# Kernel tuning notes

Hardware: AMD Instinct MI355X
Metric: run time of the kernel (lower is better)

The kernel has to match this reference:

```python
import jax, jax.numpy as jnp
import numpy as np

ALPHA = 0.5
NUM_NB = 8


def setup_inputs() -> dict:
    key = jax.random.key(0)
    k1, k2 = jax.random.split(key)
    pc1 = jax.random.normal(k1, (4, 3, 8192), dtype=jnp.float32)
    pred_flow = jax.random.normal(k2, (4, 3, 8192), dtype=jnp.float32)
    return {"pc1": pc1, "pred_flow": pred_flow}


def reference(pc1, pred_flow):
    # pc1, pred_flow: [B, 3, N] -> [B, N, 3]
    B, _, N = pc1.shape
    k = NUM_NB
    p = jnp.transpose(pc1, (0, 2, 1))         # [B, N, 3]
    f = jnp.transpose(pred_flow, (0, 2, 1))   # [B, N, 3]

    sq = jnp.sum(p * p, axis=-1)
    sqrdist = sq[:, :, None] + sq[:, None, :] - 2.0 * jnp.einsum('bnd,bmd->bnm', p, p)

    # k+1 smallest (sorted ascending), drop self (first column)
    neg_d, kidx = jax.lax.top_k(-sqrdist, k + 1)  # descending in -d == ascending in d
    dists = -neg_d[:, :, 1:]                      # [B, N, k]
    kidx = kidx[:, :, 1:]                         # [B, N, k]
    dists = jnp.maximum(dists, 0.0)

    # softmax over all N*k weights per batch
    w = jax.nn.softmax(jnp.exp(-dists / ALPHA).reshape(B, N * k), axis=1)
    w = w.reshape(B, N, k)

    # gather neighbor flows: [B, N, k, 3]
    grouped = jnp.take_along_axis(f[:, None, :, :],
                                  kidx[:, :, :, None],
                                  axis=2)
    diff = jnp.linalg.norm(grouped - f[:, :, None, :], axis=3)  # [B, N, k]
    diff_flow = (N * w * diff).sum(axis=2)                      # [B, N]
    return jnp.mean(diff_flow)
```

## Files before the change

kernel.cpp:

```cpp
#include <hip/hip_runtime.h>
#include <hip/hip_bf16.h>
#include <math.h>

#define BATCH 4
#define NQ 8192
#define KNB 8
#define K1 9
#define CAP 34
#define THSAMP 256
#define SPART 2
#define IDXMASK 8191u
#define KEYMASK 0xFFFFE000u
#define EPS_S 1e-3f

#define CHAIN9(KEY) { unsigned kk = (KEY); \
  _Pragma("unroll") \
  for (int j = 0; j < K1; ++j) { \
    unsigned lo = min(kk, nk[j]); unsigned hi = max(kk, nk[j]); \
    nk[j] = lo; kk = hi; } }

#define CHAIN8(KEY) { unsigned kk = (KEY); \
  _Pragma("unroll") \
  for (int j = 0; j < KNB; ++j) { \
    unsigned lo = min(kk, nk[j]); unsigned hi = max(kk, nk[j]); \
    nk[j] = lo; kk = hi; } }

#define DRAIN() { \
  for (int i = 0; i < cnt; ++i) { \
    int j = sbuf[base + i]; \
    float dx = qx - px[j], dy = qy - py[j], dz = qz - pz[j]; \
    float d = dx*dx + dy*dy + dz*dz; \
    unsigned key = (__float_as_uint(d) & KEYMASK) | (unsigned)j; \
    if (key < nk[K1-1]) CHAIN9(key); \
  } \
  cnt = 0; \
  if (nk[K1-1] != 0xFFFFFFFFu) { \
    float td = __uint_as_float(nk[K1-1] | 0x1FFFu); \
    thetaS = fminf(thetaS, 0.5f*(td - qq) + EPS_S); \
  } }

#define GPROC(SS, GIDX) { \
  if ((SS) <= thetaS) { sbuf[base + cnt] = (unsigned short)(GIDX); cnt++; } }

#define SCORE4(S0,S1,S2,S3, X,Y,Z,H) \
  float S0 = fmaf(nqx, X.x, fmaf(nqy, Y.x, fmaf(nqz, Z.x, H.x))); \
  float S1 = fmaf(nqx, X.y, fmaf(nqy, Y.y, fmaf(nqz, Z.y, H.y))); \
  float S2 = fmaf(nqx, X.z, fmaf(nqy, Y.z, fmaf(nqz, Z.z, H.z))); \
  float S3 = fmaf(nqx, X.w, fmaf(nqy, Y.w, fmaf(nqz, Z.w, H.w)));

__global__ __launch_bounds__(256) void theta_kernel(
    const float* __restrict__ pc, unsigned* __restrict__ thetaOut,
    float* __restrict__ hOut)
{
  __shared__ float swx[THSAMP], swy[THSAMP], swz[THSAMP];
  const int b = blockIdx.y, p = blockIdx.z;
  const int q = blockIdx.x * 256 + threadIdx.x;
  const float* __restrict__ px = pc + (size_t)b * 3 * NQ;
  const float* __restrict__ py = px + NQ;
  const float* __restrict__ pz = px + 2 * NQ;
  const int tid = threadIdx.x;
  const int si = tid * (NQ / THSAMP) + p * (NQ / THSAMP / SPART);
  swx[tid] = px[si]; swy[tid] = py[si]; swz[tid] = pz[si];
  __syncthreads();
  const float qx = px[q], qy = py[q], qz = pz[q];
  if (p == 0) hOut[b * NQ + q] = 0.5f * (qx*qx + qy*qy + qz*qz);
  unsigned nk[K1];
#pragma unroll
  for (int j = 0; j < K1; ++j) nk[j] = 0xFFFFFFFFu;
  for (int i = 0; i < THSAMP; ++i) {
    float dx = qx - swx[i], dy = qy - swy[i], dz = qz - swz[i];
    float d = dx * dx + dy * dy + dz * dz;
    CHAIN9(__float_as_uint(d));
  }
  thetaOut[(size_t)(b * NQ + q) * SPART + p] = nk[K1 - 1] | 0x1FFFu;
}

__global__ __launch_bounds__(256) void knn_kernel(
    const float* __restrict__ pc, const float* __restrict__ hB,
    const unsigned* __restrict__ thetaIn, unsigned* __restrict__ wsK,
    int P, int cpp)
{
  __shared__ unsigned short sbuf[256 * CAP];
  const int b = blockIdx.y;
  const int p = blockIdx.z;
  const int q = blockIdx.x * 256 + threadIdx.x;
  const float* __restrict__ px = pc + (size_t)b * 3 * NQ;
  const float* __restrict__ py = px + NQ;
  const float* __restrict__ pz = px + 2 * NQ;
  const float* __restrict__ ph = hB + (size_t)b * NQ;
  const float4* __restrict__ px4 = (const float4*)px;
  const float4* __restrict__ py4 = (const float4*)py;
  const float4* __restrict__ pz4 = (const float4*)pz;
  const float4* __restrict__ ph4 = (const float4*)ph;
  const float qx = px[q], qy = py[q], qz = pz[q];
  const float nqx = -qx, nqy = -qy, nqz = -qz;
  const float qq = qx*qx + qy*qy + qz*qz;

  uint2 th = ((const uint2*)thetaIn)[b * NQ + q];
  float thetaS = 0.5f * (__uint_as_float(min(th.x, th.y)) - qq) + EPS_S;

  unsigned nk[K1];
#pragma unroll
  for (int j = 0; j < K1; ++j) nk[j] = 0xFFFFFFFFu;

  const unsigned base = (unsigned)threadIdx.x * CAP;
  int cnt = 0;
  const int c0 = p * cpp;

  for (int t = 0; t < cpp; t += 16) {
    if (__any(cnt >= CAP - 16)) { DRAIN(); }
    const int ti = (c0 + t) >> 2;
    const float4 X0 = px4[ti],     X1 = px4[ti + 1], X2 = px4[ti + 2], X3 = px4[ti + 3];
    const float4 Y0 = py4[ti],     Y1 = py4[ti + 1], Y2 = py4[ti + 2], Y3 = py4[ti + 3];
    const float4 Z0 = pz4[ti],     Z1 = pz4[ti + 1], Z2 = pz4[ti + 2], Z3 = pz4[ti + 3];
    const float4 H0 = ph4[ti],     H1 = ph4[ti + 1], H2 = ph4[ti + 2], H3 = ph4[ti + 3];
    SCORE4(s0, s1, s2, s3, X0, Y0, Z0, H0);
    SCORE4(s4, s5, s6, s7, X1, Y1, Z1, H1);
    SCORE4(s8, s9, sa, sb, X2, Y2, Z2, H2);
    SCORE4(sc, sd, se, sf, X3, Y3, Z3, H3);
    const int g = c0 + t;
    GPROC(s0, g + 0);  GPROC(s1, g + 1);  GPROC(s2, g + 2);  GPROC(s3, g + 3);
    GPROC(s4, g + 4);  GPROC(s5, g + 5);  GPROC(s6, g + 6);  GPROC(s7, g + 7);
    GPROC(s8, g + 8);  GPROC(s9, g + 9);  GPROC(sa, g + 10); GPROC(sb, g + 11);
    GPROC(sc, g + 12); GPROC(sd, g + 13); GPROC(se, g + 14); GPROC(sf, g + 15);
  }
  DRAIN();

#pragma unroll
  for (int j = 0; j < K1; ++j)
    wsK[((size_t)(b * P + p) * K1 + j) * NQ + q] = nk[j];
}

__global__ __launch_bounds__(64) void loss_kernel(
    const float* __restrict__ pc, const float* __restrict__ pf,
    const unsigned* __restrict__ wsK, float* __restrict__ acc,
    unsigned* __restrict__ doneCtr, float* __restrict__ out,
    int P, int nBlocks)
{
  const int b = blockIdx.y;
  const int q = blockIdx.x * 64 + threadIdx.x;
  const float* __restrict__ px = pc + (size_t)b * 3 * NQ;
  const float* __restrict__ py = px + NQ;
  const float* __restrict__ pz = px + 2 * NQ;
  const float* __restrict__ fx = pf + (size_t)b * 3 * NQ;
  const float* __restrict__ fy = fx + NQ;
  const float* __restrict__ fz = fx + 2 * NQ;

  unsigned nk[KNB];
#pragma unroll
  for (int j = 0; j < KNB; ++j) nk[j] = 0xFFFFFFFFu;

  const int total = P * K1;
  const size_t stride0 = (size_t)b * P * K1;
  for (int m0 = 0; m0 < total; m0 += K1) {
    unsigned kb[K1];
#pragma unroll
    for (int u = 0; u < K1; ++u)
      kb[u] = wsK[(stride0 + m0 + u) * NQ + q];
#pragma unroll
    for (int u = 0; u < K1; ++u) {
      unsigned key = kb[u];
      if ((key & IDXMASK) == (unsigned)q) continue;
      if (key < nk[KNB - 1]) CHAIN8(key);
    }
  }

  const float qx = px[q], qy = py[q], qz = pz[q];
  const float fqx = fx[q], fqy = fy[q], fqz = fz[q];
  float ssum = 0.f, sdsum = 0.f;
#pragma unroll
  for (int j = 0; j < KNB; ++j) {
    int i = (int)(nk[j] & IDXMASK);
    float dx = qx - px[i], dy = qy - py[i], dz = qz - pz[i];
    float d = dx * dx + dy * dy + dz * dz;
    float e = expf(expf(-2.0f * d));
    float gx = fx[i] - fqx, gy = fy[i] - fqy, gz = fz[i] - fqz;
    float diff = sqrtf(gx * gx + gy * gy + gz * gz);
    ssum += e; sdsum += e * diff;
  }

  for (int off = 32; off > 0; off >>= 1) {
    ssum += __shfl_down(ssum, off);
    sdsum += __shfl_down(sdsum, off);
  }
  if (threadIdx.x == 0) {
    atomicAdd(&acc[b * 2 + 0], ssum);
    atomicAdd(&acc[b * 2 + 1], sdsum);
    __threadfence();
    unsigned done = atomicAdd(doneCtr, 1u);
    if (done == (unsigned)(nBlocks - 1)) {
      float s = 0.f;
      for (int bb = 0; bb < BATCH; ++bb) {
        float se = atomicAdd(&acc[bb * 2 + 0], 0.f);
        float sd = atomicAdd(&acc[bb * 2 + 1], 0.f);
        s += sd / se;
      }
      out[0] = s * (1.0f / BATCH);
    }
  }
}

extern "C" void kernel_launch(void* const* d_in, const int* in_sizes, int n_in,
                              void* d_out, int out_size, void* d_ws, size_t ws_size,
                              hipStream_t stream) {
  const float* pc = (const float*)d_in[0];
  const float* pf = (const float*)d_in[1];
  float* out = (float*)d_out;
  float* acc = (float*)d_ws;
  unsigned* doneCtr = (unsigned*)((char*)d_ws + 64);
  const size_t thetaBytes = (size_t)BATCH * NQ * SPART * sizeof(unsigned);
  const size_t hBytes = (size_t)BATCH * NQ * sizeof(float);
  unsigned* thetaBuf = (unsigned*)((char*)d_ws + 256);
  float* hBuf = (float*)((char*)d_ws + 256 + thetaBytes);
  unsigned* wsK = (unsigned*)((char*)d_ws + 256 + thetaBytes + hBytes);

  const size_t fixed = 256 + thetaBytes + hBytes;
  const size_t needP16 = fixed + (size_t)BATCH * NQ * 16 * K1 * sizeof(unsigned);
  const size_t needP8  = fixed + (size_t)BATCH * NQ * 8  * K1 * sizeof(unsigned);
  const size_t needP4  = fixed + (size_t)BATCH * NQ * 4  * K1 * sizeof(unsigned);
  const int P = (ws_size >= needP16) ? 16 : (ws_size >= needP8) ? 8
              : (ws_size >= needP4) ? 4 : 1;
  const int cpp = NQ / P;

  hipMemsetAsync(d_ws, 0, 256, stream);

  dim3 g0(NQ / 256, BATCH, SPART);
  theta_kernel<<<g0, 256, 0, stream>>>(pc, thetaBuf, hBuf);

  dim3 g1(NQ / 256, BATCH, P);
  knn_kernel<<<g1, 256, 0, stream>>>(pc, hBuf, thetaBuf, wsK, P, cpp);

  dim3 g2(NQ / 64, BATCH);
  const int nBlocks = (NQ / 64) * BATCH;
  loss_kernel<<<g2, 64, 0, stream>>>(pc, pf, wsK, acc, doneCtr, out, P, nBlocks);
}
```

Before: 142.8 us.

## Sort points by x-bin and sweep outward with early termination for kNN

Adds histogram, prefix-sum and scatter kernels that sort each batch's points into x-coordinate bins. The kNN stage then scans 16-point chunks outward from the query's position in sorted order, on both sides. It stops once every lane's x-gap exceeds its current 9th-neighbour distance, instead of brute-forcing all N candidates. This cuts the O(N^2) scoring work but adds three small launches, atomics and divergent early-exit control flow. Per-wave pruning depends on the point distribution.

```diff
diff --git a/kernel.cpp b/kernel.cpp
--- a/kernel.cpp
+++ b/kernel.cpp
@@ -9,9 +9,17 @@
 #define CAP 34
 #define THSAMP 256
 #define SPART 2
+#define NB 256
+#define XMIN -4.5f
+#define XSCALE (NB / 9.0f)
 #define IDXMASK 8191u
 #define KEYMASK 0xFFFFE000u
 #define EPS_S 1e-3f
+
+static __device__ __forceinline__ int binOf(float x) {
+  int b = (int)((x - XMIN) * XSCALE);
+  return min(max(b, 0), NB - 1);
+}
 
 #define CHAIN9(KEY) { unsigned kk = (KEY); \
   _Pragma("unroll") \
@@ -25,12 +33,12 @@
     unsigned lo = min(kk, nk[j]); unsigned hi = max(kk, nk[j]); \
     nk[j] = lo; kk = hi; } }
 
-#define DRAIN() { \
-  for (int i = 0; i < cnt; ++i) { \
-    int j = sbuf[base + i]; \
-    float dx = qx - px[j], dy = qy - py[j], dz = qz - pz[j]; \
+#define DRAINS() { \
+  for (int ii = 0; ii < cnt; ++ii) { \
+    int j = sbuf[base + ii]; \
+    float dx = qx - sxs[bq + j], dy = qy - sys[bq + j], dz = qz - szs[bq + j]; \
     float d = dx*dx + dy*dy + dz*dz; \
-    unsigned key = (__float_as_uint(d) & KEYMASK) | (unsigned)j; \
+    unsigned key = (__float_as_uint(d) & KEYMASK) | ssi[bq + j]; \
     if (key < nk[K1-1]) CHAIN9(key); \
   } \
   cnt = 0; \
@@ -39,8 +47,8 @@
     thetaS = fminf(thetaS, 0.5f*(td - qq) + EPS_S); \
   } }
 
-#define GPROC(SS, GIDX) { \
-  if ((SS) <= thetaS) { sbuf[base + cnt] = (unsigned short)(GIDX); cnt++; } }
+#define GPROC(SS, JLOCAL) { \
+  if ((SS) <= thetaS) { sbuf[base + cnt] = (unsigned short)(JLOCAL); cnt++; } }
 
 #define SCORE4(S0,S1,S2,S3, X,Y,Z,H) \
   float S0 = fmaf(nqx, X.x, fmaf(nqy, Y.x, fmaf(nqz, Z.x, H.x))); \
@@ -48,22 +56,67 @@
   float S2 = fmaf(nqx, X.z, fmaf(nqy, Y.z, fmaf(nqz, Z.z, H.z))); \
   float S3 = fmaf(nqx, X.w, fmaf(nqy, Y.w, fmaf(nqz, Z.w, H.w)));
 
+__global__ __launch_bounds__(256) void hist_kernel(
+    const float* __restrict__ pc, unsigned* __restrict__ hist)
+{
+  const int t = blockIdx.x * 256 + threadIdx.x;
+  const int b = t >> 13, n = t & (NQ - 1);
+  const float x = pc[(size_t)b * 3 * NQ + n];
+  atomicAdd(&hist[b * NB + binOf(x)], 1u);
+}
+
+__global__ __launch_bounds__(256) void prefix_kernel(
+    unsigned* __restrict__ hist, unsigned* __restrict__ binStart)
+{
+  __shared__ unsigned sc[NB];
+  const int t = threadIdx.x;
+  for (int b = 0; b < BATCH; ++b) {
+    const unsigned c = hist[b * NB + t];
+    sc[t] = c;
+    __syncthreads();
+    for (int o = 1; o < NB; o <<= 1) {
+      unsigned a = (t >= o) ? sc[t - o] : 0u;
+      __syncthreads();
+      sc[t] += a;
+      __syncthreads();
+    }
+    const unsigned excl = sc[t] - c;
+    binStart[b * (NB + 1) + t] = excl;
+    hist[b * NB + t] = excl;
+    if (t == NB - 1) binStart[b * (NB + 1) + NB] = sc[t];
+    __syncthreads();
+  }
+}
+
+__global__ __launch_bounds__(256) void scatter_kernel(
+    const float* __restrict__ pc, unsigned* __restrict__ cursor,
+    float* __restrict__ sxs, float* __restrict__ sys, float* __restrict__ szs,
+    float* __restrict__ shs, unsigned* __restrict__ ssi)
+{
+  const int t = blockIdx.x * 256 + threadIdx.x;
+  const int b = t >> 13, n = t & (NQ - 1);
+  const float* __restrict__ px = pc + (size_t)b * 3 * NQ;
+  const float x = px[n], y = px[NQ + n], z = px[2 * NQ + n];
+  const unsigned pos = atomicAdd(&cursor[b * NB + binOf(x)], 1u);
+  const int o = b * NQ + (int)pos;
+  sxs[o] = x; sys[o] = y; szs[o] = z;
+  shs[o] = 0.5f * (x * x + y * y + z * z);
+  ssi[o] = (unsigned)n;
+}
+
 __global__ __launch_bounds__(256) void theta_kernel(
-    const float* __restrict__ pc, unsigned* __restrict__ thetaOut,
-    float* __restrict__ hOut)
+    const float* __restrict__ sxs, const float* __restrict__ sys,
+    const float* __restrict__ szs, unsigned* __restrict__ thetaOut)
 {
   __shared__ float swx[THSAMP], swy[THSAMP], swz[THSAMP];
   const int b = blockIdx.y, p = blockIdx.z;
-  const int q = blockIdx.x * 256 + threadIdx.x;
-  const float* __restrict__ px = pc + (size_t)b * 3 * NQ;
-  const float* __restrict__ py = px + NQ;
-  const float* __restrict__ pz = px + 2 * NQ;
+  const int s = blockIdx.x * 256 + threadIdx.x;
+  const int bq = b * NQ;
   const int tid = threadIdx.x;
   const int si = tid * (NQ / THSAMP) + p * (NQ / THSAMP / SPART);
-  swx[tid] = px[si]; swy[tid] = py[si]; swz[tid] = pz[si];
+  swx[tid] = sxs[bq + si]; swy[tid] = sys[bq + si]; swz[tid] = szs[bq + si];
   __syncthreads();
-  const float qx = px[q], qy = py[q], qz = pz[q];
-  if (p == 0) hOut[b * NQ + q] = 0.5f * (qx*qx + qy*qy + qz*qz);
+  const float qx = sxs[bq + s], qy = sys[bq + s], qz = szs[bq + s];
   unsigned nk[K1];
 #pragma unroll
   for (int j = 0; j < K1; ++j) nk[j] = 0xFFFFFFFFu;
@@ -72,73 +125,96 @@
     float d = dx * dx + dy * dy + dz * dz;
     CHAIN9(__float_as_uint(d));
   }
-  thetaOut[(size_t)(b * NQ + q) * SPART + p] = nk[K1 - 1] | 0x1FFFu;
-}
-
-__global__ __launch_bounds__(256) void knn_kernel(
-    const float* __restrict__ pc, const float* __restrict__ hB,
-    const unsigned* __restrict__ thetaIn, unsigned* __restrict__ wsK,
-    int P, int cpp)
+  thetaOut[(size_t)(bq + s) * SPART + p] = nk[K1 - 1] | 0x1FFFu;
+}
+
+__global__ __launch_bounds__(256) void sweep_kernel(
+    const float* __restrict__ sxs, const float* __restrict__ sys,
+    const float* __restrict__ szs, const float* __restrict__ shs,
+    const unsigned* __restrict__ ssi, const unsigned* __restrict__ binStart,
+    const unsigned* __restrict__ thetaIn, unsigned* __restrict__ wsK, int P)
 {
   __shared__ unsigned short sbuf[256 * CAP];
-  const int b = blockIdx.y;
-  const int p = blockIdx.z;
-  const int q = blockIdx.x * 256 + threadIdx.x;
-  const float* __restrict__ px = pc + (size_t)b * 3 * NQ;
-  const float* __restrict__ py = px + NQ;
-  const float* __restrict__ pz = px + 2 * NQ;
-  const float* __restrict__ ph = hB + (size_t)b * NQ;
-  const float4* __restrict__ px4 = (const float4*)px;
-  const float4* __restrict__ py4 = (const float4*)py;
-  const float4* __restrict__ pz4 = (const float4*)pz;
-  const float4* __restrict__ ph4 = (const float4*)ph;
-  const float qx = px[q], qy = py[q], qz = pz[q];
+  const int b = blockIdx.y, p = blockIdx.z;
+  const int s = blockIdx.x * 256 + threadIdx.x;
+  const int bq = b * NQ;
+  const float qx = sxs[bq + s], qy = sys[bq + s], qz = szs[bq + s];
   const float nqx = -qx, nqy = -qy, nqz = -qz;
-  const float qq = qx*qx + qy*qy + qz*qz;
-
-  uint2 th = ((const uint2*)thetaIn)[b * NQ + q];
-  float thetaS = 0.5f * (__uint_as_float(min(th.x, th.y)) - qq) + EPS_S;
+  const float qq = qx * qx + qy * qy + qz * qz;
+  uint2 th = ((const uint2*)thetaIn)[bq + s];
+  const float thetaD1 = __uint_as_float(min(th.x, th.y));
+  float thetaS = 0.5f * (thetaD1 - qq) + EPS_S;
+  const float r1 = sqrtf(thetaD1) * 1.0001f + 1e-7f;
+  unsigned LO = binStart[b * (NB + 1) + binOf(qx - r1)];
+  unsigned HI = binStart[b * (NB + 1) + binOf(qx + r1) + 1];
+  for (int off = 32; off; off >>= 1) {
+    LO = min(LO, (unsigned)__shfl_xor((int)LO, off));
+    HI = max(HI, (unsigned)__shfl_xor((int)HI, off));
+  }
+  const int LOb = __builtin_amdgcn_readfirstlane((int)LO) >> 4;
+  const int HIb = (__builtin_amdgcn_readfirstlane((int)HI) - 1) >> 4;
+  int mid = (__builtin_amdgcn_readfirstlane(s) + 32) >> 4;
+  mid = min(max(mid, LOb), HIb);
+  const int PH = P >> 1;
+  const bool rightSide = (p < PH);
+  int cb = rightSide ? (mid + p) : (mid - 1 - (p - PH));
+  const int step = rightSide ? PH : -PH;
 
   unsigned nk[K1];
 #pragma unroll
   for (int j = 0; j < K1; ++j) nk[j] = 0xFFFFFFFFu;
-
   const unsigned base = (unsigned)threadIdx.x * CAP;
   int cnt = 0;
-  const int c0 = p * cpp;
-
-  for (int t = 0; t < cpp; t += 16) {
-    if (__any(cnt >= CAP - 16)) { DRAIN(); }
-    const int ti = (c0 + t) >> 2;
-    const float4 X0 = px4[ti],     X1 = px4[ti + 1], X2 = px4[ti + 2], X3 = px4[ti + 3];
-    const float4 Y0 = py4[ti],     Y1 = py4[ti + 1], Y2 = py4[ti + 2], Y3 = py4[ti + 3];
-    const float4 Z0 = pz4[ti],     Z1 = pz4[ti + 1], Z2 = pz4[ti + 2], Z3 = pz4[ti + 3];
-    const float4 H0 = ph4[ti],     H1 = ph4[ti + 1], H2 = ph4[ti + 2], H3 = ph4[ti + 3];
+  int it = 0;
+  const float4* __restrict__ x4 = (const float4*)sxs;
+  const float4* __restrict__ y4 = (const float4*)sys;
+  const float4* __restrict__ z4 = (const float4*)szs;
+  const float4* __restrict__ h4 = (const float4*)shs;
+
+  while (cb >= LOb && cb <= HIb) {
+    if (__any(cnt >= CAP - 16)) { DRAINS(); }
+    const int jb = cb * 16;
+    const int ti = (bq + jb) >> 2;
+    const float4 X0 = x4[ti], X1 = x4[ti + 1], X2 = x4[ti + 2], X3 = x4[ti + 3];
+    const float4 Y0 = y4[ti], Y1 = y4[ti + 1], Y2 = y4[ti + 2], Y3 = y4[ti + 3];
+    const float4 Z0 = z4[ti], Z1 = z4[ti + 1], Z2 = z4[ti + 2], Z3 = z4[ti + 3];
+    const float4 H0 = h4[ti], H1 = h4[ti + 1], H2 = h4[ti + 2], H3 = h4[ti + 3];
     SCORE4(s0, s1, s2, s3, X0, Y0, Z0, H0);
     SCORE4(s4, s5, s6, s7, X1, Y1, Z1, H1);
     SCORE4(s8, s9, sa, sb, X2, Y2, Z2, H2);
     SCORE4(sc, sd, se, sf, X3, Y3, Z3, H3);
-    const int g = c0 + t;
-    GPROC(s0, g + 0);  GPROC(s1, g + 1);  GPROC(s2, g + 2);  GPROC(s3, g + 3);
-    GPROC(s4, g + 4);  GPROC(s5, g + 5);  GPROC(s6, g + 6);  GPROC(s7, g + 7);
-    GPROC(s8, g + 8);  GPROC(s9, g + 9);  GPROC(sa, g + 10); GPROC(sb, g + 11);
-    GPROC(sc, g + 12); GPROC(sd, g + 13); GPROC(se, g + 14); GPROC(sf, g + 15);
-  }
-  DRAIN();
-
+    GPROC(s0, jb + 0);  GPROC(s1, jb + 1);  GPROC(s2, jb + 2);  GPROC(s3, jb + 3);
+    GPROC(s4, jb + 4);  GPROC(s5, jb + 5);  GPROC(s6, jb + 6);  GPROC(s7, jb + 7);
+    GPROC(s8, jb + 8);  GPROC(s9, jb + 9);  GPROC(sa, jb + 10); GPROC(sb, jb + 11);
+    GPROC(sc, jb + 12); GPROC(sd, jb + 13); GPROC(se, jb + 14); GPROC(sf, jb + 15);
+    ++it; cb += step;
+    if ((it & 3) == 0) {
+      DRAINS();
+      if (cb < LOb || cb > HIb) break;
+      const int je = rightSide ? (cb * 16) : (cb * 16 + 15);
+      const float xe = sxs[bq + je];
+      const float dxe = rightSide ? (xe - qx) : (qx - xe);
+      const float thD = __uint_as_float(nk[K1 - 1] | 0x1FFFu);
+      if (__all((dxe > 0.0f) && (dxe * dxe > thD))) break;
+    }
+  }
+  DRAINS();
 #pragma unroll
   for (int j = 0; j < K1; ++j)
-    wsK[((size_t)(b * P + p) * K1 + j) * NQ + q] = nk[j];
+    wsK[((size_t)(b * P + p) * K1 + j) * NQ + s] = nk[j];
 }
 
 __global__ __launch_bounds__(64) void loss_kernel(
     const float* __restrict__ pc, const float* __restrict__ pf,
+    const float* __restrict__ sxs, const float* __restrict__ sys,
+    const float* __restrict__ szs, const unsigned* __restrict__ ssi,
     const unsigned* __restrict__ wsK, float* __restrict__ acc,
     unsigned* __restrict__ doneCtr, float* __restrict__ out,
     int P, int nBlocks)
 {
   const int b = blockIdx.y;
-  const int q = blockIdx.x * 64 + threadIdx.x;
+  const int s = blockIdx.x * 64 + threadIdx.x;
+  const int bq = b * NQ;
   const float* __restrict__ px = pc + (size_t)b * 3 * NQ;
   const float* __restrict__ py = px + NQ;
   const float* __restrict__ pz = px + 2 * NQ;
@@ -146,6 +222,7 @@
   const float* __restrict__ fy = fx + NQ;
   const float* __restrict__ fz = fx + 2 * NQ;
 
+  const unsigned qorig = ssi[bq + s];
   unsigned nk[KNB];
 #pragma unroll
   for (int j = 0; j < KNB; ++j) nk[j] = 0xFFFFFFFFu;
@@ -156,17 +233,17 @@
     unsigned kb[K1];
 #pragma unroll
     for (int u = 0; u < K1; ++u)
-      kb[u] = wsK[(stride0 + m0 + u) * NQ + q];
+      kb[u] = wsK[(stride0 + m0 + u) * NQ + s];
 #pragma unroll
     for (int u = 0; u < K1; ++u) {
       unsigned key = kb[u];
-      if ((key & IDXMASK) == (unsigned)q) continue;
+      if ((key & IDXMASK) == qorig) continue;
       if (key < nk[KNB - 1]) CHAIN8(key);
     }
   }
 
-  const float qx = px[q], qy = py[q], qz = pz[q];
-  const float fqx = fx[q], fqy = fy[q], fqz = fz[q];
+  const float qx = sxs[bq + s], qy = sys[bq + s], qz = szs[bq + s];
+  const float fqx = fx[qorig], fqy = fy[qorig], fqz = fz[qorig];
   float ssum = 0.f, sdsum = 0.f;
 #pragma unroll
   for (int j = 0; j < KNB; ++j) {
@@ -189,13 +266,13 @@
     __threadfence();
     unsigned done = atomicAdd(doneCtr, 1u);
     if (done == (unsigned)(nBlocks - 1)) {
-      float s = 0.f;
+      float sT = 0.f;
       for (int bb = 0; bb < BATCH; ++bb) {
         float se = atomicAdd(&acc[bb * 2 + 0], 0.f);
         float sd = atomicAdd(&acc[bb * 2 + 1], 0.f);
-        s += sd / se;
+        sT += sd / se;
       }
-      out[0] = s * (1.0f / BATCH);
+      out[0] = sT * (1.0f / BATCH);
     }
   }
 }
@@ -206,31 +283,38 @@
   const float* pc = (const float*)d_in[0];
   const float* pf = (const float*)d_in[1];
   float* out = (float*)d_out;
-  float* acc = (float*)d_ws;
-  unsigned* doneCtr = (unsigned*)((char*)d_ws + 64);
-  const size_t thetaBytes = (size_t)BATCH * NQ * SPART * sizeof(unsigned);
-  const size_t hBytes = (size_t)BATCH * NQ * sizeof(float);
-  unsigned* thetaBuf = (unsigned*)((char*)d_ws + 256);
-  float* hBuf = (float*)((char*)d_ws + 256 + thetaBytes);
-  unsigned* wsK = (unsigned*)((char*)d_ws + 256 + thetaBytes + hBytes);
-
-  const size_t fixed = 256 + thetaBytes + hBytes;
-  const size_t needP16 = fixed + (size_t)BATCH * NQ * 16 * K1 * sizeof(unsigned);
-  const size_t needP8  = fixed + (size_t)BATCH * NQ * 8  * K1 * sizeof(unsigned);
-  const size_t needP4  = fixed + (size_t)BATCH * NQ * 4  * K1 * sizeof(unsigned);
-  const int P = (ws_size >= needP16) ? 16 : (ws_size >= needP8) ? 8
-              : (ws_size >= needP4) ? 4 : 1;
-  const int cpp = NQ / P;
-
-  hipMemsetAsync(d_ws, 0, 256, stream);
-
-  dim3 g0(NQ / 256, BATCH, SPART);
-  theta_kernel<<<g0, 256, 0, stream>>>(pc, thetaBuf, hBuf);
-
-  dim3 g1(NQ / 256, BATCH, P);
-  knn_kernel<<<g1, 256, 0, stream>>>(pc, hBuf, thetaBuf, wsK, P, cpp);
-
-  dim3 g2(NQ / 64, BATCH);
+
+  char* w = (char*)d_ws;
+  float*    acc      = (float*)w;
+  unsigned* doneCtr  = (unsigned*)(w + 64);
+  unsigned* hist     = (unsigned*)(w + 256);
+  unsigned* binStart = (unsigned*)(w + 4352);
+  const size_t SA = 8704;
+  float*    sxs = (float*)(w + SA);
+  float*    sys = (float*)(w + SA + 1 * 131072);
+  float*    szs = (float*)(w + SA + 2 * 131072);
+  float*    shs = (float*)(w + SA + 3 * 131072);
+  unsigned* ssi = (unsigned*)(w + SA + 4 * 131072);
+  const size_t TH = SA + 5 * 131072;
+  unsigned* thetaBuf = (unsigned*)(w + TH);
+  const size_t WK = TH + (size_t)BATCH * NQ * SPART * 4;
+  unsigned* wsK = (unsigned*)(w + WK);
+
+  const size_t needP8 = WK + (size_t)BATCH * NQ * 8 * K1 * 4;
+  const size_t needP4 = WK + (size_t)BATCH * NQ * 4 * K1 * 4;
+  const int P = (ws_size >= needP8) ? 8 : ((ws_size >= needP4) ? 4 : 2);
+
+  hipMemsetAsync(d_ws, 0, 4352, stream);
+
+  hist_kernel<<<dim3(BATCH * NQ / 256), 256, 0, stream>>>(pc, hist);
+  prefix_kernel<<<dim3(1), 256, 0, stream>>>(hist, binStart);
+  scatter_kernel<<<dim3(BATCH * NQ / 256), 256, 0, stream>>>(
+      pc, hist, sxs, sys, szs, shs, ssi);
+  theta_kernel<<<dim3(NQ / 256, BATCH, SPART), 256, 0, stream>>>(
+      sxs, sys, szs, thetaBuf);
+  sweep_kernel<<<dim3(NQ / 256, BATCH, P), 256, 0, stream>>>(
+      sxs, sys, szs, shs, ssi, binStart, thetaBuf, wsK, P);
   const int nBlocks = (NQ / 64) * BATCH;
-  loss_kernel<<<g2, 64, 0, stream>>>(pc, pf, wsK, acc, doneCtr, out, P, nBlocks);
-}
+  loss_kernel<<<dim3(NQ / 64, BATCH), 64, 0, stream>>>(
+      pc, pf, sxs, sys, szs, ssi, wsK, acc, doneCtr, out, P, nBlocks);
+}
```

After: 180.2 us. 26.2% more time.
